# Kernel tuning notes

Measured on AMD Instinct MI355X. Metric: run time of the kernel, lower is better.

The kernel has to match this reference:

```python
import jax, jax.numpy as jnp
import numpy as np

NEG_BIG = -9e15

def setup_inputs() -> dict:
    key = jax.random.key(0)
    kx, ka, kW, k1, k2 = jax.random.split(key, 5)
    B, N, F, H, D = 8, 1024, 1024, 16, 64
    x = jax.random.normal(kx, (B, N, F), dtype=jnp.float32)
    adj = jax.random.randint(ka, (B, N, N), 0, 2, dtype=jnp.int32)
    # xavier_uniform with gain=1.414
    gain = 1.414
    limW = gain * np.sqrt(6.0 / (F + D))
    lima = gain * np.sqrt(6.0 / (D + 1))
    W = jax.random.uniform(kW, (H, F, D), minval=-limW, maxval=limW, dtype=jnp.float32)
    a1 = jax.random.uniform(k1, (H, D), minval=-lima, maxval=lima, dtype=jnp.float32)
    a2 = jax.random.uniform(k2, (H, D), minval=-lima, maxval=lima, dtype=jnp.float32)
    return {"x": x, "adj": adj, "W": W, "a1": a1, "a2": a2}

def reference(x, adj, W, a1, a2):
    alpha = 0.2
    # Wh: [B, H, N, D]
    Wh = jnp.einsum('bnf,hfd->bhnd', x, W)
    f1 = jnp.einsum('bhnd,hd->bhn', Wh, a1)  # [B,H,N]
    f2 = jnp.einsum('bhnd,hd->bhn', Wh, a2)  # [B,H,N]
    e = f1[:, :, :, None] + f2[:, :, None, :]          # [B,H,N,N]
    e = jnp.where(e > 0, e, alpha * e)                  # leaky relu
    mask = (adj > 0)[:, None, :, :]                     # [B,1,N,N]
    scores = jnp.where(mask, e, NEG_BIG)
    attn = jax.nn.softmax(scores, axis=-1)              # [B,H,N,N]
    # dropout omitted (inference / training=False)
    h_prime = jnp.einsum('bhnm,bhmd->bhnd', attn, Wh)   # [B,H,N,D]
    B, H, N, D = h_prime.shape
    # concat heads along feature dim (matches torch.cat over dim=2)
    y = jnp.transpose(h_prime, (0, 2, 1, 3)).reshape(B, N, H * D)
    return y
```

## Files before the change

kernel.cpp:

```cpp
#include <hip/hip_runtime.h>

typedef float    f32x4 __attribute__((ext_vector_type(4)));
typedef short    s16x8 __attribute__((ext_vector_type(8)));
typedef _Float16 f16x8 __attribute__((ext_vector_type(8)));
typedef _Float16 f16x4 __attribute__((ext_vector_type(4)));
typedef unsigned int   u32x4 __attribute__((ext_vector_type(4)));


__device__ __forceinline__ unsigned short bf16rne(float f){
  unsigned u = __float_as_uint(f);
  return (unsigned short)((u + 0x7FFFu + ((u >> 16) & 1u)) >> 16);
}

__global__ __launch_bounds__(256) void prep_kernel(const int* __restrict__ adj,
    const float* __restrict__ x, const float* __restrict__ W,
    unsigned* __restrict__ maskb, unsigned short* __restrict__ xb,
    unsigned short* __restrict__ Wt)
{
  const int bid = blockIdx.x, tid = threadIdx.x;
  if (bid < 1024) {
    const int lane = tid & 63;
    int gw = (bid * 256 + tid) >> 6;
    for (int s = gw; s < 131072; s += 4096) {
      int a = adj[(size_t)s * 64 + lane];
      unsigned long long m = __ballot(a > 0);
      if (lane == 0) {
        maskb[s * 2]     = (unsigned)m;
        maskb[s * 2 + 1] = (unsigned)(m >> 32);
      }
    }
  } else if (bid < 5120) {
    int idx = ((bid - 1024) * 256 + tid) * 8;
    f32x4 v0 = *reinterpret_cast<const f32x4*>(&x[idx]);
    f32x4 v1 = *reinterpret_cast<const f32x4*>(&x[idx + 4]);
    u32x4 o;
    o[0] = (unsigned)bf16rne(v0[0]) | ((unsigned)bf16rne(v0[1]) << 16);
    o[1] = (unsigned)bf16rne(v0[2]) | ((unsigned)bf16rne(v0[3]) << 16);
    o[2] = (unsigned)bf16rne(v1[0]) | ((unsigned)bf16rne(v1[1]) << 16);
    o[3] = (unsigned)bf16rne(v1[2]) | ((unsigned)bf16rne(v1[3]) << 16);
    *reinterpret_cast<u32x4*>(&xb[idx]) = o;
  } else {
    __shared__ float t[16][17];
    int rel = bid - 5120;
    int f0 = (rel & 63) * 16, d0 = ((rel >> 6) & 3) * 16, hh = rel >> 8;
    const int tx = tid & 15, ty = tid >> 4;
    t[ty][tx] = W[(size_t)hh * 65536 + (size_t)(f0 + ty) * 64 + (d0 + tx)];
    __syncthreads();
    float v = t[tx][ty];
    size_t o = (size_t)(hh * 64 + d0 + ty) * 1024 + (f0 + tx);
    Wt[o] = bf16rne(v);
  }
}

__global__ __launch_bounds__(256, 3) void gemm_kernel(const unsigned short* __restrict__ xb,
    const unsigned short* __restrict__ Btg,
    const float* __restrict__ a1, const float* __restrict__ a2,
    _Float16* __restrict__ WhT, float* __restrict__ f1, float* __restrict__ f2)
{
  __shared__ unsigned short Ah[128 * 40], Bh[128 * 40];
  const int tid  = threadIdx.x;
  const int lane = tid & 63, wave = tid >> 6;
  const int m0 = blockIdx.x * 128, n0 = blockIdx.y * 128;
  const int wm = (wave & 1) * 64, wn = (wave >> 1) * 64;
  const int rA = lane & 15, kg = lane >> 4;

  f32x4 acc[4][4] = {};

  for (int k0 = 0; k0 < 1024; k0 += 32) {
#pragma unroll
    for (int r = 0; r < 2; ++r) {
      int flat = r * 256 + tid;
      int row = flat >> 2;
      int o8  = (flat & 3) << 3;
      *reinterpret_cast<u32x4*>(&Ah[row * 40 + o8]) =
          *reinterpret_cast<const u32x4*>(&xb[(size_t)(m0 + row) * 1024 + k0 + o8]);
    }
#pragma unroll
    for (int r = 0; r < 2; ++r) {
      int flat = r * 256 + tid;
      int row = flat >> 2;
      int o8  = (flat & 3) << 3;
      *reinterpret_cast<u32x4*>(&Bh[row * 40 + o8]) =
          *reinterpret_cast<const u32x4*>(&Btg[(size_t)(n0 + row) * 1024 + k0 + o8]);
    }
    __syncthreads();

    s16x8 ah[4], bh[4];
#pragma unroll
    for (int i = 0; i < 4; ++i)
      ah[i] = *reinterpret_cast<const s16x8*>(&Ah[(wm + i * 16 + rA) * 40 + kg * 8]);
#pragma unroll
    for (int j = 0; j < 4; ++j)
      bh[j] = *reinterpret_cast<const s16x8*>(&Bh[(wn + j * 16 + rA) * 40 + kg * 8]);
#pragma unroll
    for (int i = 0; i < 4; ++i)
#pragma unroll
      for (int j = 0; j < 4; ++j)
        acc[i][j] = __builtin_amdgcn_mfma_f32_16x16x32_bf16(ah[i], bh[j], acc[i][j], 0, 0, 0);
    __syncthreads();
  }

#pragma unroll
  for (int i = 0; i < 4; ++i) {
    int gm0 = m0 + wm + i * 16 + kg * 4;
#pragma unroll
    for (int j = 0; j < 4; ++j) {
      int gn = n0 + wn + j * 16 + rA;
      int bb = gm0 >> 10, nn = gm0 & 1023;
      int hh = gn >> 6,  dd = gn & 63;
      f16x4 hv;
#pragma unroll
      for (int jj = 0; jj < 4; ++jj) hv[jj] = (_Float16)acc[i][j][jj];
      *reinterpret_cast<f16x4*>(&WhT[((size_t)((bb * 16 + hh) * 64 + dd) << 10) + nn]) = hv;
    }
  }

  const int hw = (n0 + wn) >> 6;
  float a1v[4], a2v[4];
#pragma unroll
  for (int j = 0; j < 4; ++j) {
    int d = j * 16 + rA;
    a1v[j] = a1[hw * 64 + d];
    a2v[j] = a2[hw * 64 + d];
  }
#pragma unroll
  for (int i = 0; i < 4; ++i) {
#pragma unroll
    for (int jj = 0; jj < 4; ++jj) {
      float s1 = 0.f, s2 = 0.f;
#pragma unroll
      for (int j = 0; j < 4; ++j) {
        float v = acc[i][j][jj];
        s1 += v * a1v[j];
        s2 += v * a2v[j];
      }
#pragma unroll
      for (int off = 1; off < 16; off <<= 1) {
        s1 += __shfl_xor(s1, off);
        s2 += __shfl_xor(s2, off);
      }
      if (rA == 0) {
        int gm = m0 + wm + i * 16 + kg * 4 + jj;
        int bb = gm >> 10, nn = gm & 1023;
        size_t o = (size_t)(bb * 16 + hw) * 1024 + nn;
        f1[o] = s1;
        f2[o] = s2;
      }
    }
  }
}

__global__ __launch_bounds__(256, 4) void pv_kernel(const _Float16* __restrict__ WhT,
    const float* __restrict__ f1, const float* __restrict__ f2,
    const unsigned* __restrict__ maskb, float* __restrict__ y)
{
  const int tid = threadIdx.x, lane = tid & 63, wave = tid >> 6;
  const int rb = blockIdx.x, h = blockIdx.y, b = blockIdx.z;
  const int bh = b * 16 + h;
  const int n0 = rb * 128;
  const _Float16* whtb = WhT + ((size_t)bh << 16);

  __shared__ _Float16 Bsh[64 * 72];
  __shared__ float Cs[1024], Ds[1024];
  __shared__ float smx[4];
  __shared__ unsigned long long lutm[16];

  const float K = 1.44269504f;

  float pmax;
  {
    f32x4 fv = *reinterpret_cast<const f32x4*>(&f2[(size_t)bh * 1024 + tid * 4]);
    f32x4 sv, cv, dv;
#pragma unroll
    for (int e = 0; e < 4; ++e) {
      sv[e] = fv[e] * K;
      cv[e] = __builtin_amdgcn_exp2f(sv[e]);
      dv[e] = __builtin_amdgcn_exp2f(0.2f * sv[e]);
    }
    *reinterpret_cast<f32x4*>(&Cs[tid * 4]) = cv;
    *reinterpret_cast<f32x4*>(&Ds[tid * 4]) = dv;
    pmax = fmaxf(fmaxf(sv[0], sv[1]), fmaxf(sv[2], sv[3]));
  }
#pragma unroll
  for (int off = 32; off; off >>= 1) pmax = fmaxf(pmax, __shfl_xor(pmax, off));
  if (lane == 0) smx[wave] = pmax;
  if (tid < 16) {
    unsigned lo = ((tid & 1) ? 0xFFFFu : 0u) | ((tid & 2) ? 0xFFFF0000u : 0u);
    unsigned hi = ((tid & 4) ? 0xFFFFu : 0u) | ((tid & 8) ? 0xFFFF0000u : 0u);
    lutm[tid] = ((unsigned long long)hi << 32) | lo;
  }
  __syncthreads();

  const float m2s = fmaxf(fmaxf(smx[0], smx[1]), fmaxf(smx[2], smx[3]));

  const int rA = lane & 15, kg = lane >> 4;
  const int wrow = wave * 32;
  f32x4 acc[2][4] = {};
  f32x4 dacc[2] = {};
  int   rloc[2];
  float At[2], Bt[2];
  const unsigned* mrow[2];
#pragma unroll
  for (int t = 0; t < 2; ++t) {
    rloc[t] = wrow + t * 16 + rA;
    float f1p = f1[(size_t)bh * 1024 + n0 + rloc[t]] * K;
    float sf = f1p + m2s;
    float Mp = fmaxf(sf, 0.2f * sf);
    At[t] = __builtin_amdgcn_exp2f(f1p - Mp);
    Bt[t] = __builtin_amdgcn_exp2f(0.2f * f1p - Mp);
    mrow[t] = maskb + ((size_t)(b << 10) + n0 + rloc[t]) * 32;
  }
  f16x8 ones;
#pragma unroll
  for (int e = 0; e < 8; ++e) ones[e] = (_Float16)1.0f;

  for (int m0 = 0; m0 < 1024; m0 += 64) {
    uint2 mw2[2];
#pragma unroll
    for (int t = 0; t < 2; ++t)
      mw2[t] = *reinterpret_cast<const uint2*>(&mrow[t][m0 >> 5]);
#pragma unroll
    for (int r = 0; r < 2; ++r) {
      int flat = r * 256 + tid;
      int d = flat >> 3, o = (flat & 7) << 3;
      *reinterpret_cast<u32x4*>(&Bsh[d * 72 + o]) =
          *reinterpret_cast<const u32x4*>(&whtb[(size_t)d * 1024 + m0 + o]);
    }
    __syncthreads();
#pragma unroll
    for (int ks = 0; ks < 2; ++ks) {
      const int kc = m0 + ks * 32 + kg * 8;
      f32x4 ca = *reinterpret_cast<const f32x4*>(&Cs[kc]);
      f32x4 cb = *reinterpret_cast<const f32x4*>(&Cs[kc + 4]);
      f32x4 da = *reinterpret_cast<const f32x4*>(&Ds[kc]);
      f32x4 db = *reinterpret_cast<const f32x4*>(&Ds[kc + 4]);
      f16x8 pa[2];
#pragma unroll
      for (int t = 0; t < 2; ++t) {
        unsigned mw = (&mw2[t].x)[ks] >> (kg * 8);
        f16x8 pt;
#pragma unroll
        for (int jj = 0; jj < 8; ++jj) {
          float C = (jj < 4) ? ca[jj] : cb[jj - 4];
          float D = (jj < 4) ? da[jj] : db[jj - 4];
          pt[jj] = (_Float16)fmaxf(At[t] * C, Bt[t] * D);
        }
        u32x4 pw = __builtin_bit_cast(u32x4, pt);
        unsigned long long mq0 = lutm[mw & 15u];
        unsigned long long mq1 = lutm[(mw >> 4) & 15u];
        pw[0] &= (unsigned)mq0;  pw[1] &= (unsigned)(mq0 >> 32);
        pw[2] &= (unsigned)mq1;  pw[3] &= (unsigned)(mq1 >> 32);
        pa[t] = __builtin_bit_cast(f16x8, pw);
        dacc[t] = __builtin_amdgcn_mfma_f32_16x16x32_f16(pa[t], ones, dacc[t], 0, 0, 0);
      }
#pragma unroll
      for (int j = 0; j < 4; ++j) {
        f16x8 bf = *reinterpret_cast<const f16x8*>(&Bsh[(j * 16 + rA) * 72 + ks * 32 + kg * 8]);
        acc[0][j] = __builtin_amdgcn_mfma_f32_16x16x32_f16(pa[0], bf, acc[0][j], 0, 0, 0);
        acc[1][j] = __builtin_amdgcn_mfma_f32_16x16x32_f16(pa[1], bf, acc[1][j], 0, 0, 0);
      }
    }
    __syncthreads();
  }

#pragma unroll
  for (int t = 0; t < 2; ++t) {
    f32x4 rd;
#pragma unroll
    for (int jj = 0; jj < 4; ++jj) rd[jj] = dacc[t][jj] > 0.f ? 1.0f / dacc[t][jj] : 0.f;
#pragma unroll
    for (int j = 0; j < 4; ++j) {
#pragma unroll
      for (int jj = 0; jj < 4; ++jj) {
        int row = wrow + t * 16 + kg * 4 + jj;
        int n = n0 + row, d = j * 16 + rA;
        y[(((size_t)b * 1024 + n) << 10) + h * 64 + d] = acc[t][j][jj] * rd[jj];
      }
    }
  }
}

extern "C" void kernel_launch(void* const* d_in, const int* in_sizes, int n_in,
                              void* d_out, int out_size, void* d_ws, size_t ws_size,
                              hipStream_t stream)
{
  const float* x  = (const float*)d_in[0];
  const int*   adj = (const int*)d_in[1];
  const float* W  = (const float*)d_in[2];
  const float* a1 = (const float*)d_in[3];
  const float* a2 = (const float*)d_in[4];
  float* y = (float*)d_out;

  char* ws = (char*)d_ws;
  unsigned short* Wt = (unsigned short*)(ws);
  unsigned*       maskb = (unsigned*)(ws + ((size_t)2 << 20));
  float* f1   = (float*)(ws + ((size_t)3 << 20));
  float* f2   = (float*)(ws + ((size_t)3 << 20) + ((size_t)512 << 10));
  _Float16* WhT = (_Float16*)(ws + ((size_t)4 << 20));
  unsigned short* xb = (unsigned short*)(ws + ((size_t)20 << 20));

  prep_kernel<<<9216, 256, 0, stream>>>(adj, x, W, maskb, xb, Wt);
  gemm_kernel<<<dim3(64, 8), 256, 0, stream>>>(xb, Wt, a1, a2, WhT, f1, f2);
  pv_kernel<<<dim3(8, 16, 8), 256, 0, stream>>>(WhT, f1, f2, maskb, y);
}
```

Baseline: 94.29 us.

## Double-buffer shared-memory tiles in GEMM and PV kernels

```diff
diff --git a/kernel.cpp b/kernel.cpp
--- a/kernel.cpp
+++ b/kernel.cpp
@@ -52,12 +52,26 @@
   }
 }
 
+#define GSTAGE(BUF, K0) { \
+  _Pragma("unroll") \
+  for (int r = 0; r < 2; ++r) { \
+    int flat = r * 256 + tid; int row = flat >> 2; int o8 = (flat & 3) << 3; \
+    *reinterpret_cast<u32x4*>(&Ah[BUF][row * 40 + o8]) = \
+        *reinterpret_cast<const u32x4*>(&xb[(size_t)(m0 + row) * 1024 + (K0) + o8]); \
+  } \
+  _Pragma("unroll") \
+  for (int r = 0; r < 2; ++r) { \
+    int flat = r * 256 + tid; int row = flat >> 2; int o8 = (flat & 3) << 3; \
+    *reinterpret_cast<u32x4*>(&Bh[BUF][row * 40 + o8]) = \
+        *reinterpret_cast<const u32x4*>(&Btg[(size_t)(n0 + row) * 1024 + (K0) + o8]); \
+  } }
+
 __global__ __launch_bounds__(256, 3) void gemm_kernel(const unsigned short* __restrict__ xb,
     const unsigned short* __restrict__ Btg,
     const float* __restrict__ a1, const float* __restrict__ a2,
     _Float16* __restrict__ WhT, float* __restrict__ f1, float* __restrict__ f2)
 {
-  __shared__ unsigned short Ah[128 * 40], Bh[128 * 40];
+  __shared__ unsigned short Ah[2][128 * 40], Bh[2][128 * 40];
   const int tid  = threadIdx.x;
   const int lane = tid & 63, wave = tid >> 6;
   const int m0 = blockIdx.x * 128, n0 = blockIdx.y * 128;
@@ -66,38 +80,26 @@
 
   f32x4 acc[4][4] = {};
 
+  GSTAGE(0, 0);
+  __syncthreads();
+  int cur = 0;
   for (int k0 = 0; k0 < 1024; k0 += 32) {
-#pragma unroll
-    for (int r = 0; r < 2; ++r) {
-      int flat = r * 256 + tid;
-      int row = flat >> 2;
-      int o8  = (flat & 3) << 3;
-      *reinterpret_cast<u32x4*>(&Ah[row * 40 + o8]) =
-          *reinterpret_cast<const u32x4*>(&xb[(size_t)(m0 + row) * 1024 + k0 + o8]);
-    }
-#pragma unroll
-    for (int r = 0; r < 2; ++r) {
-      int flat = r * 256 + tid;
-      int row = flat >> 2;
-      int o8  = (flat & 3) << 3;
-      *reinterpret_cast<u32x4*>(&Bh[row * 40 + o8]) =
-          *reinterpret_cast<const u32x4*>(&Btg[(size_t)(n0 + row) * 1024 + k0 + o8]);
-    }
-    __syncthreads();
+    if (k0 + 32 < 1024) { GSTAGE(cur ^ 1, k0 + 32); }
 
     s16x8 ah[4], bh[4];
 #pragma unroll
     for (int i = 0; i < 4; ++i)
-      ah[i] = *reinterpret_cast<const s16x8*>(&Ah[(wm + i * 16 + rA) * 40 + kg * 8]);
+      ah[i] = *reinterpret_cast<const s16x8*>(&Ah[cur][(wm + i * 16 + rA) * 40 + kg * 8]);
 #pragma unroll
     for (int j = 0; j < 4; ++j)
-      bh[j] = *reinterpret_cast<const s16x8*>(&Bh[(wn + j * 16 + rA) * 40 + kg * 8]);
+      bh[j] = *reinterpret_cast<const s16x8*>(&Bh[cur][(wn + j * 16 + rA) * 40 + kg * 8]);
 #pragma unroll
     for (int i = 0; i < 4; ++i)
 #pragma unroll
       for (int j = 0; j < 4; ++j)
         acc[i][j] = __builtin_amdgcn_mfma_f32_16x16x32_bf16(ah[i], bh[j], acc[i][j], 0, 0, 0);
     __syncthreads();
+    cur ^= 1;
   }
 
 #pragma unroll
@@ -149,6 +151,14 @@
     }
   }
 }
+
+#define PSTAGE(BUF, M0) { \
+  _Pragma("unroll") \
+  for (int r = 0; r < 2; ++r) { \
+    int flat = r * 256 + tid; int d = flat >> 3; int o = (flat & 7) << 3; \
+    *reinterpret_cast<u32x4*>(&Bsh[BUF][d * 72 + o]) = \
+        *reinterpret_cast<const u32x4*>(&whtb[(size_t)d * 1024 + (M0) + o]); \
+  } }
 
 __global__ __launch_bounds__(256, 4) void pv_kernel(const _Float16* __restrict__ WhT,
     const float* __restrict__ f1, const float* __restrict__ f2,
@@ -160,7 +170,7 @@
   const int n0 = rb * 128;
   const _Float16* whtb = WhT + ((size_t)bh << 16);
 
-  __shared__ _Float16 Bsh[64 * 72];
+  __shared__ _Float16 Bsh[2][64 * 72];
   __shared__ float Cs[1024], Ds[1024];
   __shared__ float smx[4];
   __shared__ unsigned long long lutm[16];
@@ -214,19 +224,21 @@
 #pragma unroll
   for (int e = 0; e < 8; ++e) ones[e] = (_Float16)1.0f;
 
+  uint2 mwcur[2], mwnext[2];
+#pragma unroll
+  for (int t = 0; t < 2; ++t)
+    mwcur[t] = *reinterpret_cast<const uint2*>(&mrow[t][0]);
+  PSTAGE(0, 0);
+  __syncthreads();
+  int cur = 0;
+
   for (int m0 = 0; m0 < 1024; m0 += 64) {
-    uint2 mw2[2];
-#pragma unroll
-    for (int t = 0; t < 2; ++t)
-      mw2[t] = *reinterpret_cast<const uint2*>(&mrow[t][m0 >> 5]);
-#pragma unroll
-    for (int r = 0; r < 2; ++r) {
-      int flat = r * 256 + tid;
-      int d = flat >> 3, o = (flat & 7) << 3;
-      *reinterpret_cast<u32x4*>(&Bsh[d * 72 + o]) =
-          *reinterpret_cast<const u32x4*>(&whtb[(size_t)d * 1024 + m0 + o]);
-    }
-    __syncthreads();
+    if (m0 + 64 < 1024) {
+      PSTAGE(cur ^ 1, m0 + 64);
+#pragma unroll
+      for (int t = 0; t < 2; ++t)
+        mwnext[t] = *reinterpret_cast<const uint2*>(&mrow[t][(m0 + 64) >> 5]);
+    }
 #pragma unroll
     for (int ks = 0; ks < 2; ++ks) {
       const int kc = m0 + ks * 32 + kg * 8;
@@ -237,7 +249,7 @@
       f16x8 pa[2];
 #pragma unroll
       for (int t = 0; t < 2; ++t) {
-        unsigned mw = (&mw2[t].x)[ks] >> (kg * 8);
+        unsigned mw = (&mwcur[t].x)[ks] >> (kg * 8);
         f16x8 pt;
 #pragma unroll
         for (int jj = 0; jj < 8; ++jj) {
@@ -255,12 +267,15 @@
       }
 #pragma unroll
       for (int j = 0; j < 4; ++j) {
-        f16x8 bf = *reinterpret_cast<const f16x8*>(&Bsh[(j * 16 + rA) * 72 + ks * 32 + kg * 8]);
+        f16x8 bf = *reinterpret_cast<const f16x8*>(&Bsh[cur][(j * 16 + rA) * 72 + ks * 32 + kg * 8]);
         acc[0][j] = __builtin_amdgcn_mfma_f32_16x16x32_f16(pa[0], bf, acc[0][j], 0, 0, 0);
         acc[1][j] = __builtin_amdgcn_mfma_f32_16x16x32_f16(pa[1], bf, acc[1][j], 0, 0, 0);
       }
     }
     __syncthreads();
+    cur ^= 1;
+#pragma unroll
+    for (int t = 0; t < 2; ++t) mwcur[t] = mwnext[t];
   }
 
 #pragma unroll
```

Result: no change. 93.23 us (-1.1%).
